# Kernel optimization log

Measured on AMD Instinct MI355X. Metric: run time of the kernel, lower is better.

The kernel has to match this reference:

```python
import jax, jax.numpy as jnp
import numpy as np


def _pairwise_l2(set1, set2):
    # set1: [B, N, C], set2: [B, M, C] -> [B, N, M] Euclidean distances.
    # Equivalent to ||a - b||_2 computed via the expanded quadratic form,
    # avoiding the O(B*N*M*C) broadcasted-difference intermediate.
    sq1 = jnp.sum(set1 * set1, axis=-1)  # [B, N]
    sq2 = jnp.sum(set2 * set2, axis=-1)  # [B, M]
    inner = jnp.einsum('bnc,bmc->bnm', set1, set2)  # [B, N, M]
    d2 = sq1[:, :, None] + sq2[:, None, :] - 2.0 * inner
    return jnp.sqrt(jnp.maximum(d2, 0.0))


def reference(set1, set2):
    # mode == Hausdorff.average
    if set1.ndim == 2:
        set1 = set1[None]
    if set2.ndim == 2:
        set2 = set2[None]
    distances = _pairwise_l2(set1, set2)  # [B, N, M]
    term_1 = jnp.mean(jnp.min(distances, axis=2), axis=1)  # [B]
    term_2 = jnp.mean(jnp.min(distances, axis=1), axis=1)  # [B]
    res = term_1 + term_2
    if res.shape[0] == 1:
        res = jnp.squeeze(res, axis=0)
    return res


def setup_inputs() -> dict:
    key = jax.random.key(0)
    k1, k2 = jax.random.split(key)
    B, N, M, C = 8, 4096, 4096, 128
    set1 = jax.random.normal(k1, (B, N, C), dtype=jnp.float32)
    set2 = jax.random.normal(k2, (B, M, C), dtype=jnp.float32)
    return {"set1": set1, "set2": set2}
```

## Files before the change

kernel.cpp:

```cpp
#include <hip/hip_runtime.h>

#define B_ 8
#define N_ 4096
#define M_ 4096
#define C_ 128
#define BN_ (B_ * N_)
#define BM_ (B_ * M_)

typedef __attribute__((ext_vector_type(8))) short bf16x8;
typedef __attribute__((ext_vector_type(4))) float floatx4;
typedef __attribute__((ext_vector_type(8))) unsigned short ushort8;

__device__ __forceinline__ unsigned short f2bf(float x) {
    unsigned int u = __float_as_uint(x);
    u += 0x7FFFu + ((u >> 16) & 1u);
    return (unsigned short)(u >> 16);
}


__global__ __launch_bounds__(256) void prep_kernel(
    const float* __restrict__ S1, const float* __restrict__ S2,
    unsigned int* __restrict__ minbuf, float* __restrict__ norms,
    unsigned short* __restrict__ Afrag, unsigned short* __restrict__ Bfrag) {
    const int lane = threadIdx.x & 63;
    const int w    = threadIdx.x >> 6;
    const int lm   = lane & 15;
    const int quad = lane >> 4;

    const int unit  = blockIdx.x * 4 + w;
    const int batch = unit >> 9;
    const int rem   = unit & 511;
    const int isB   = rem >> 8;
    const int q     = rem & 255;
    const int t     = q >> 2;
    const int h     = (q >> 1) & 1;
    const int j     = q & 1;
    const int m     = t * 64 + h * 32 + j * 16 + lm;

    const float* src = (isB ? S2 : S1) + ((size_t)batch * 4096 + m) * C_;
    unsigned short* dst = (isB ? Bfrag : Afrag) + (size_t)batch * (4096 * C_)
                        + (size_t)(((t * 2 + h) * 2 + j) * 4) * 64 * 8;

    float s = 0.f;
    #pragma unroll
    for (int c = 0; c < 4; ++c) {
        float4 v0 = *(const float4*)(src + c * 32 + quad * 8);
        float4 v1 = *(const float4*)(src + c * 32 + quad * 8 + 4);
        s += v0.x*v0.x + v0.y*v0.y + v0.z*v0.z + v0.w*v0.w
           + v1.x*v1.x + v1.y*v1.y + v1.z*v1.z + v1.w*v1.w;
        ushort8 o;
        o[0] = f2bf(v0.x); o[1] = f2bf(v0.y); o[2] = f2bf(v0.z); o[3] = f2bf(v0.w);
        o[4] = f2bf(v1.x); o[5] = f2bf(v1.y); o[6] = f2bf(v1.z); o[7] = f2bf(v1.w);
        *(ushort8*)&dst[(size_t)(c * 64 + lane) * 8] = o;
    }
    s += __shfl_xor(s, 16, 64);
    s += __shfl_xor(s, 32, 64);
    if (quad == 0) {
        const int gr = (isB ? BN_ : 0) + batch * 4096 + m;
        norms[gr]  = s;
        minbuf[gr] = 0x7F800000u;
    }
}

__global__ __launch_bounds__(256, 2) void hausdorff_mfma(
    const unsigned short* __restrict__ Afrag, const unsigned short* __restrict__ Bfrag,
    const float* __restrict__ asq_g, const float* __restrict__ bsq_g,
    unsigned int* __restrict__ rowmin, unsigned int* __restrict__ colmin) {

    const int b     = blockIdx.z;
    const int row0  = blockIdx.x * 128;
    const int panel = blockIdx.y;
    const int tid   = threadIdx.x;
    const int lane  = tid & 63;
    const int w     = tid >> 6;
    const int lm    = lane & 15;
    const int quad  = lane >> 4;
    const int wrow  = (w >> 1) * 64;
    const int wch   = w & 1;

    const unsigned short* Af = Afrag + (size_t)b * (4096 * C_);
    const unsigned short* Bf = Bfrag + (size_t)b * (4096 * C_);
    const int tA  = (row0 >> 6) + (w >> 1);
    const int tB0 = panel * 16;

    bf16x8 af[4][4];
    #pragma unroll
    for (int i = 0; i < 4; ++i)
        #pragma unroll
        for (int c = 0; c < 4; ++c)
            af[i][c] = *(const bf16x8*)
                &Af[(size_t)(((((tA * 2 + (i >> 1)) * 2 + (i & 1)) * 4 + c) * 64 + lane)) * 8];

    float sah[16];
    #pragma unroll
    for (int i = 0; i < 4; ++i) {
        float4 t = *(const float4*)&asq_g[(size_t)b * N_ + row0 + wrow + 16 * i + 4 * quad];
        sah[4*i+0] = -0.5f * t.x; sah[4*i+1] = -0.5f * t.y;
        sah[4*i+2] = -0.5f * t.z; sah[4*i+3] = -0.5f * t.w;
    }

    float rv[16];
    #pragma unroll
    for (int v = 0; v < 16; ++v) rv[v] = -1e30f;

    auto loadB = [&](bf16x8 (&d)[2][4], int it) {
        const unsigned short* base =
            &Bf[(size_t)(((tB0 + it) * 2 + wch) * 2) * 4 * 64 * 8];
        #pragma unroll
        for (int j = 0; j < 2; ++j)
            #pragma unroll
            for (int c = 0; c < 4; ++c)
                d[j][c] = *(const bf16x8*)&base[(size_t)((j * 4 + c) * 64 + lane) * 8];
    };

    auto loadSb = [&](float& n0, float& n1, int it) {
        const int colbase = panel * 1024 + it * 64 + wch * 32;
        n0 = -0.5f * bsq_g[(size_t)b * M_ + colbase + lm];
        n1 = -0.5f * bsq_g[(size_t)b * M_ + colbase + 16 + lm];
    };

    auto compute = [&](bf16x8 (&bfr)[2][4], int it, float nb0, float nb1) {
        const int colbase = panel * 1024 + it * 64 + wch * 32;

        floatx4 acc[4][2];
        #pragma unroll
        for (int i = 0; i < 4; ++i)
            #pragma unroll
            for (int reg = 0; reg < 4; ++reg) {
                acc[i][0][reg] = sah[4*i+reg] + nb0;
                acc[i][1][reg] = sah[4*i+reg] + nb1;
            }

        #pragma unroll
        for (int c = 0; c < 4; ++c)
            #pragma unroll
            for (int i = 0; i < 4; ++i)
                #pragma unroll
                for (int j = 0; j < 2; ++j)
                    acc[i][j] = __builtin_amdgcn_mfma_f32_16x16x32_bf16(
                        af[i][c], bfr[j][c], acc[i][j], 0, 0, 0);

        float cv0 = -1e30f, cv1 = -1e30f;
        #pragma unroll
        for (int i = 0; i < 4; ++i)
            #pragma unroll
            for (int reg = 0; reg < 4; ++reg) {
                const int v = 4 * i + reg;
                rv[v] = fmaxf(rv[v], fmaxf(acc[i][0][reg], acc[i][1][reg]));
                cv0 = fmaxf(cv0, acc[i][0][reg]);
                cv1 = fmaxf(cv1, acc[i][1][reg]);
            }
        cv0 = fmaxf(cv0, __shfl_xor(cv0, 16, 64));
        cv0 = fmaxf(cv0, __shfl_xor(cv0, 32, 64));
        cv1 = fmaxf(cv1, __shfl_xor(cv1, 16, 64));
        cv1 = fmaxf(cv1, __shfl_xor(cv1, 32, 64));
        if (quad == 0) {
            atomicMin(&colmin[(size_t)b * M_ + colbase + lm],
                      __float_as_uint(fmaxf(-2.0f * cv0, 0.f)));
            atomicMin(&colmin[(size_t)b * M_ + colbase + 16 + lm],
                      __float_as_uint(fmaxf(-2.0f * cv1, 0.f)));
        }
    };

    bf16x8 bfP[2][4], bfQ[2][4];
    float nbP0, nbP1, nbQ0, nbQ1;
    loadB(bfP, 0);
    loadSb(nbP0, nbP1, 0);
    for (int it2 = 0; it2 < 16; it2 += 2) {
        loadB(bfQ, it2 + 1);
        loadSb(nbQ0, nbQ1, it2 + 1);
        compute(bfP, it2, nbP0, nbP1);
        if (it2 < 14) {
            loadB(bfP, it2 + 2);
            loadSb(nbP0, nbP1, it2 + 2);
        }
        compute(bfQ, it2 + 1, nbQ0, nbQ1);
    }

    #pragma unroll
    for (int s = 1; s < 16; s <<= 1)
        #pragma unroll
        for (int v = 0; v < 16; ++v)
            rv[v] = fmaxf(rv[v], __shfl_xor(rv[v], s, 64));
    if (lm == 0) {
        #pragma unroll
        for (int v = 0; v < 16; ++v)
            atomicMin(&rowmin[(size_t)b * N_ + row0 + wrow + 16 * (v >> 2) +
                              4 * quad + (v & 3)],
                      __float_as_uint(fmaxf(-2.0f * rv[v], 0.f)));
    }
}

__global__ __launch_bounds__(256) void hausdorff_reduce(
    const unsigned int* __restrict__ rowmin,
    const unsigned int* __restrict__ colmin, float* __restrict__ out) {
    __shared__ float ws4[4];
    const int b = blockIdx.x;
    float s = 0.f;
    for (int i = threadIdx.x; i < N_; i += 256)
        s += sqrtf(fmaxf(__uint_as_float(rowmin[(size_t)b * N_ + i]), 0.f)) * (1.f / N_)
           + sqrtf(fmaxf(__uint_as_float(colmin[(size_t)b * M_ + i]), 0.f)) * (1.f / M_);
    #pragma unroll
    for (int off = 32; off > 0; off >>= 1) s += __shfl_down(s, off, 64);
    if ((threadIdx.x & 63) == 0) ws4[threadIdx.x >> 6] = s;
    __syncthreads();
    if (threadIdx.x == 0)
        out[b] = ws4[0] + ws4[1] + ws4[2] + ws4[3];
}

extern "C" void kernel_launch(void* const* d_in, const int* in_sizes, int n_in,
                              void* d_out, int out_size, void* d_ws, size_t ws_size,
                              hipStream_t stream) {
    const float* s1 = (const float*)d_in[0];
    const float* s2 = (const float*)d_in[1];
    float* out = (float*)d_out;

    unsigned int* rowmin  = (unsigned int*)d_ws;
    unsigned int* colmin  = rowmin + BN_;
    float* norms          = (float*)(colmin + BM_);
    unsigned short* Afrag = (unsigned short*)(norms + BN_ + BM_);
    unsigned short* Bfrag = Afrag + (size_t)BN_ * C_;

    prep_kernel<<<1024, 256, 0, stream>>>(s1, s2, rowmin, norms, Afrag, Bfrag);

    dim3 grid(N_ / 128, M_ / 1024, B_);
    hausdorff_mfma<<<grid, 256, 0, stream>>>(
        Afrag, Bfrag, norms, norms + BN_, rowmin, colmin);

    hausdorff_reduce<<<B_, 256, 0, stream>>>(rowmin, colmin, out);
}
```

Measured before the change: 126.1 us.

## Replace column atomicMin with per-partition partial buffers and parallelize final reduce

The MFMA kernel no longer does global atomicMin on column minima. Each row-partition writes its column partials to a dedicated slice of a 64-way partial buffer, and the reduce kernel takes the min across the 64 partitions. The reduce is also split into 8 segments per batch, combined with atomicAdd into an output zeroed in prep. This removes contended atomics from the hot loop but adds about 8 MB of partial-buffer writes and reads plus extra workspace.

```diff
diff --git a/kernel.cpp b/kernel.cpp
--- a/kernel.cpp
+++ b/kernel.cpp
@@ -21,7 +21,8 @@
 __global__ __launch_bounds__(256) void prep_kernel(
     const float* __restrict__ S1, const float* __restrict__ S2,
     unsigned int* __restrict__ minbuf, float* __restrict__ norms,
-    unsigned short* __restrict__ Afrag, unsigned short* __restrict__ Bfrag) {
+    unsigned short* __restrict__ Afrag, unsigned short* __restrict__ Bfrag,
+    float* __restrict__ out) {
     const int lane = threadIdx.x & 63;
     const int w    = threadIdx.x >> 6;
     const int lm   = lane & 15;
@@ -58,14 +59,15 @@
     if (quad == 0) {
         const int gr = (isB ? BN_ : 0) + batch * 4096 + m;
         norms[gr]  = s;
-        minbuf[gr] = 0x7F800000u;
-    }
+        if (!isB) minbuf[gr] = 0x7F800000u;
+    }
+    if (blockIdx.x == 0 && threadIdx.x < B_) out[threadIdx.x] = 0.f;
 }
 
 __global__ __launch_bounds__(256, 2) void hausdorff_mfma(
     const unsigned short* __restrict__ Afrag, const unsigned short* __restrict__ Bfrag,
     const float* __restrict__ asq_g, const float* __restrict__ bsq_g,
-    unsigned int* __restrict__ rowmin, unsigned int* __restrict__ colmin) {
+    unsigned int* __restrict__ rowmin, float* __restrict__ colpart) {
 
     const int b     = blockIdx.z;
     const int row0  = blockIdx.x * 128;
@@ -77,6 +79,7 @@
     const int quad  = lane >> 4;
     const int wrow  = (w >> 1) * 64;
     const int wch   = w & 1;
+    const int part  = blockIdx.x * 2 + (w >> 1);
 
     const unsigned short* Af = Afrag + (size_t)b * (4096 * C_);
     const unsigned short* Bf = Bfrag + (size_t)b * (4096 * C_);
@@ -155,10 +158,9 @@
         cv1 = fmaxf(cv1, __shfl_xor(cv1, 16, 64));
         cv1 = fmaxf(cv1, __shfl_xor(cv1, 32, 64));
         if (quad == 0) {
-            atomicMin(&colmin[(size_t)b * M_ + colbase + lm],
-                      __float_as_uint(fmaxf(-2.0f * cv0, 0.f)));
-            atomicMin(&colmin[(size_t)b * M_ + colbase + 16 + lm],
-                      __float_as_uint(fmaxf(-2.0f * cv1, 0.f)));
+            float* dst = &colpart[((size_t)part * B_ + b) * M_ + colbase];
+            dst[lm]      = fmaxf(-2.0f * cv0, 0.f);
+            dst[16 + lm] = fmaxf(-2.0f * cv1, 0.f);
         }
     };
 
@@ -192,20 +194,28 @@
 }
 
 __global__ __launch_bounds__(256) void hausdorff_reduce(
-    const unsigned int* __restrict__ rowmin,
-    const unsigned int* __restrict__ colmin, float* __restrict__ out) {
+    const unsigned int* __restrict__ rowmin, const float* __restrict__ colpart,
+    float* __restrict__ out) {
     __shared__ float ws4[4];
-    const int b = blockIdx.x;
+    const int b    = blockIdx.x >> 3;
+    const int seg  = blockIdx.x & 7;
+    const int base = seg * 512;
     float s = 0.f;
-    for (int i = threadIdx.x; i < N_; i += 256)
-        s += sqrtf(fmaxf(__uint_as_float(rowmin[(size_t)b * N_ + i]), 0.f)) * (1.f / N_)
-           + sqrtf(fmaxf(__uint_as_float(colmin[(size_t)b * M_ + i]), 0.f)) * (1.f / M_);
+    for (int i = base + threadIdx.x; i < base + 512; i += 256)
+        s += sqrtf(fmaxf(__uint_as_float(rowmin[(size_t)b * N_ + i]), 0.f)) * (1.f / N_);
+    for (int c = base + threadIdx.x; c < base + 512; c += 256) {
+        float m = 1e30f;
+        #pragma unroll 4
+        for (int p = 0; p < 64; ++p)
+            m = fminf(m, colpart[((size_t)p * B_ + b) * M_ + c]);
+        s += sqrtf(m) * (1.f / M_);
+    }
     #pragma unroll
     for (int off = 32; off > 0; off >>= 1) s += __shfl_down(s, off, 64);
     if ((threadIdx.x & 63) == 0) ws4[threadIdx.x >> 6] = s;
     __syncthreads();
     if (threadIdx.x == 0)
-        out[b] = ws4[0] + ws4[1] + ws4[2] + ws4[3];
+        atomicAdd(&out[b], ws4[0] + ws4[1] + ws4[2] + ws4[3]);
 }
 
 extern "C" void kernel_launch(void* const* d_in, const int* in_sizes, int n_in,
@@ -216,16 +226,16 @@
     float* out = (float*)d_out;
 
     unsigned int* rowmin  = (unsigned int*)d_ws;
-    unsigned int* colmin  = rowmin + BN_;
-    float* norms          = (float*)(colmin + BM_);
+    float* norms          = (float*)(rowmin + BN_);
     unsigned short* Afrag = (unsigned short*)(norms + BN_ + BM_);
     unsigned short* Bfrag = Afrag + (size_t)BN_ * C_;
-
-    prep_kernel<<<1024, 256, 0, stream>>>(s1, s2, rowmin, norms, Afrag, Bfrag);
+    float* colpart        = (float*)(Bfrag + (size_t)BM_ * C_);
+
+    prep_kernel<<<1024, 256, 0, stream>>>(s1, s2, rowmin, norms, Afrag, Bfrag, out);
 
     dim3 grid(N_ / 128, M_ / 1024, B_);
     hausdorff_mfma<<<grid, 256, 0, stream>>>(
-        Afrag, Bfrag, norms, norms + BN_, rowmin, colmin);
-
-    hausdorff_reduce<<<B_, 256, 0, stream>>>(rowmin, colmin, out);
-}
+        Afrag, Bfrag, norms, norms + BN_, rowmin, colpart);
+
+    hausdorff_reduce<<<B_ * 8, 256, 0, stream>>>(rowmin, colpart, out);
+}
```

Measured after the change: 140.2 us. +11.2%, slower.
